# Optimization experiments

Hardware: AMD Instinct MI355X
Metric: run time of the kernel (lower is better)

## Reference

```python
import jax, jax.numpy as jnp
import numpy as np
import math

LN_EPS = 1e-5

def _ln(x, g, b):
    m = jnp.mean(x, -1, keepdims=True)
    v = jnp.mean((x - m) ** 2, -1, keepdims=True)
    return (x - m) / jnp.sqrt(v + LN_EPS) * g + b

def setup_inputs() -> dict:
    key = jax.random.key(0)
    ks = jax.random.split(key, 16)
    B, N, D, V = 2, 512, 128, 16
    w = lambda k, shape: jax.random.normal(k, shape, jnp.float32) * 0.02
    return {
        "scalar": jax.random.normal(ks[0], (B, N, D), jnp.float32),
        "vector": jax.random.normal(ks[1], (B, N, 3, V), jnp.float32),
        "coords": jax.random.normal(ks[2], (B, N, 3), jnp.float32),
        "w_q": w(ks[3], (D, D)), "b_q": jnp.zeros((D,), jnp.float32),
        "w_k": w(ks[4], (D, D)), "b_k": jnp.zeros((D,), jnp.float32),
        "w_v": w(ks[5], (D, D)), "b_v": jnp.zeros((D,), jnp.float32),
        "w_d1": w(ks[6], (1, D)), "b_d1": jnp.zeros((D,), jnp.float32),
        "w_d2": w(ks[7], (D, D)), "b_d2": jnp.zeros((D,), jnp.float32),
        "w_g": w(ks[8], (D, V)), "b_g": jnp.zeros((V,), jnp.float32),
        "w_o": w(ks[9], (D, D)), "b_o": jnp.zeros((D,), jnp.float32),
        "w_f1": w(ks[10], (D, 2 * D)), "b_f1": jnp.zeros((2 * D,), jnp.float32),
        "w_f2": w(ks[11], (2 * D, D)), "b_f2": jnp.zeros((D,), jnp.float32),
        "w_vo": w(ks[12], (V, V)), "b_vo": jnp.zeros((V,), jnp.float32),
        "g_s": jnp.ones((D,), jnp.float32), "be_s": jnp.zeros((D,), jnp.float32),
        "g_v": jnp.ones((V,), jnp.float32), "be_v": jnp.zeros((V,), jnp.float32),
    }

def reference(scalar, vector, coords, w_q, b_q, w_k, b_k, w_v, b_v,
              w_d1, b_d1, w_d2, b_d2, w_g, b_g, w_o, b_o,
              w_f1, b_f1, w_f2, b_f2, w_vo, b_vo, g_s, be_s, g_v, be_v):
    D = scalar.shape[-1]
    # pairwise geometry: [B,N,N,3], [B,N,N,1]
    rel = coords[:, :, None, :] - coords[:, None, :, :]
    dist = jnp.linalg.norm(rel, axis=-1, keepdims=True)
    direction = rel / jnp.maximum(dist, 1e-6)
    sn = _ln(scalar, g_s, be_s)
    q = sn @ w_q + b_q
    k = sn @ w_k + b_k
    v = sn @ w_v + b_v
    # distance-conditioned bias: [B,N,N,D]
    bias = jax.nn.gelu(dist @ w_d1 + b_d1, approximate=False) @ w_d2 + b_d2
    # q_i . (k_j + bias_ij) / sqrt(D)
    logits = (jnp.einsum('bid,bjd->bij', q, k)
              + jnp.einsum('bid,bijd->bij', q, bias)) / math.sqrt(D)
    attn = jax.nn.softmax(logits, axis=-1)
    # sum_j attn_ij * (v_j + bias_ij)
    upd = jnp.einsum('bij,bjd->bid', attn, v) + jnp.einsum('bij,bijd->bid', attn, bias)
    scalar = scalar + (upd @ w_o + b_o)
    h = _ln(scalar, g_s, be_s)
    scalar = scalar + (jax.nn.gelu(h @ w_f1 + b_f1, approximate=False) @ w_f2 + b_f2)
    gate = jax.nn.sigmoid(scalar @ w_g + b_g)  # [B,N,V]
    # sum_j attn_ij * (vector_j + dir_ij * gate_i) decomposed (same math, no BxNxNx3xV tensor)
    agg = (jnp.einsum('bij,bjcv->bicv', attn, vector)
           + jnp.einsum('bij,bijc->bic', attn, direction)[..., None] * gate[:, :, None, :])
    projected = _ln(agg, g_v, be_v) @ w_vo + b_vo
    return scalar, vector + projected
```

## Files before the change

kernel.cpp:

```cpp
#include <hip/hip_runtime.h>
#include <math.h>

#define D 128
#define F 256
#define V 16
#define NSEQ 512
#define NROW 1024
#define MQ 7

__device__ __forceinline__ float gelu_exact(float x) {
    return 0.5f * x * (1.0f + erff(x * 0.70710678118654752f));
}

__device__ __forceinline__ float waveSum(float v) {
#pragma unroll
    for (int o = 32; o; o >>= 1) v += __shfl_xor(v, o);
    return v;
}
__device__ __forceinline__ float waveMax(float v) {
#pragma unroll
    for (int o = 32; o; o >>= 1) v = fmaxf(v, __shfl_xor(v, o));
    return v;
}

__device__ __forceinline__ void build_A(const float* __restrict__ w_d1,
                                        const float* __restrict__ b_d1,
                                        float* A_s, int t) {
    if (t < D) {
        const float gam[MQ] = {0.f, 0.5f, 0.39894228f, 0.f, -0.06649038f, 0.f,
                               0.0099735570f};
        float w = w_d1[t], b = b_d1[t];
        float wp[MQ], bp[MQ];
        wp[0] = 1.f; bp[0] = 1.f;
#pragma unroll
        for (int i = 1; i < MQ; i++) { wp[i] = wp[i - 1] * w; bp[i] = bp[i - 1] * b; }
        float A[MQ];
#pragma unroll
        for (int m = 0; m < MQ; m++) A[m] = 0.f;
#pragma unroll
        for (int k = 1; k < MQ; k++) {
            float g = gam[k];
            if (g == 0.f) continue;
            float C = 1.f;
            for (int m = 0; m <= k; m++) {
                A[m] = fmaf(g * C, wp[m] * bp[k - m], A[m]);
                C = C * (float)(k - m) / (float)(m + 1);
            }
        }
#pragma unroll
        for (int m = 0; m < MQ; m++) A_s[t * MQ + m] = A[m];
    }
}

__global__ __launch_bounds__(1024) void k1_qkv(
    const float* __restrict__ scalar,
    const float* __restrict__ w_q, const float* __restrict__ b_q,
    const float* __restrict__ w_k, const float* __restrict__ b_k,
    const float* __restrict__ w_v, const float* __restrict__ b_v,
    const float* __restrict__ w_d1, const float* __restrict__ b_d1,
    const float* __restrict__ w_d2,
    const float* __restrict__ g_s, const float* __restrict__ be_s,
    float* __restrict__ qg, float* __restrict__ kTg, float* __restrict__ vg,
    float* __restrict__ Gg)
{
    const int t = threadIdx.x, h = t >> 8, u = t & 255, d = u & 127;
    const int w = t >> 6, ln = t & 63;
    const int r0 = blockIdx.x * 4, r = r0 + h;
    __shared__ float sn_s[4][D];
    __shared__ float k_s[4][D];
    __shared__ float pq[8][4][D], pk[8][4][D], pv[8][4][D];
    __shared__ float redA[16], redB[16];

    float x = scalar[(size_t)r * D + d];
    {
        float s = waveSum(x);
        if (ln == 0) redA[w] = s;
    }
    __syncthreads();
    float mean = (redA[4 * h] + redA[4 * h + 1] + redA[4 * h + 2] + redA[4 * h + 3])
               * (1.0f / 256.0f);
    float dv = x - mean;
    {
        float s = waveSum(dv * dv);
        if (ln == 0) redB[w] = s;
    }
    __syncthreads();
    float var = (redB[4 * h] + redB[4 * h + 1] + redB[4 * h + 2] + redB[4 * h + 3])
              * (1.0f / 256.0f);
    sn_s[h][d] = dv * rsqrtf(var + 1e-5f) * g_s[d] + be_s[d];
    __syncthreads();

    {
        const int eo = t >> 7, l = t & 127, e0 = eo * 16;
        float aq[4] = {0, 0, 0, 0}, ak[4] = {0, 0, 0, 0}, av[4] = {0, 0, 0, 0};
#pragma unroll 4
        for (int e = e0; e < e0 + 16; e++) {
            float wq = w_q[e * D + l], wk = w_k[e * D + l], wv = w_v[e * D + l];
#pragma unroll
            for (int rr = 0; rr < 4; rr++) {
                float s = sn_s[rr][e];
                aq[rr] = fmaf(s, wq, aq[rr]);
                ak[rr] = fmaf(s, wk, ak[rr]);
                av[rr] = fmaf(s, wv, av[rr]);
            }
        }
#pragma unroll
        for (int rr = 0; rr < 4; rr++) {
            pq[eo][rr][l] = aq[rr];
            pk[eo][rr][l] = ak[rr];
            pv[eo][rr][l] = av[rr];
        }
    }
    __syncthreads();

    for (int idx = t; idx < 1536; idx += 1024) {
        const int mat = idx >> 9, h2 = (idx >> 7) & 3, l = idx & 127;
        const float* P = (mat == 0) ? &pq[0][0][0]
                       : (mat == 1) ? &pk[0][0][0] : &pv[0][0][0];
        float acc = 0.f;
#pragma unroll
        for (int eo = 0; eo < 8; eo++) acc += P[(eo * 4 + h2) * D + l];
        if (mat == 0)      qg[(size_t)(r0 + h2) * D + l] = acc + b_q[l];
        else if (mat == 1) k_s[h2][l] = acc + b_k[l];
        else               vg[(size_t)(r0 + h2) * D + l] = acc + b_v[l];
    }
    __syncthreads();

    if (t < 512) kTg[(size_t)(t >> 2) * NROW + r0 + (t & 3)] = k_s[t & 3][t >> 2];

    if (blockIdx.x == 0) {
        float* A_s = &pq[0][0][0];
        build_A(w_d1, b_d1, A_s, t);
        __syncthreads();
        if (t < D * MQ) {
            const int m = t >> 7, l = t & 127;
            float acc = 0.f;
#pragma unroll 4
            for (int e = 0; e < D; e++)
                acc = fmaf(w_d2[e * D + l], A_s[e * MQ + m], acc);
            Gg[l * MQ + m] = acc;
        }
    }
}

__global__ __launch_bounds__(1024) void k23(
    const float* __restrict__ coords, const float* __restrict__ vecin,
    const float* __restrict__ scalar,
    const float* __restrict__ qg, const float* __restrict__ kTg,
    const float* __restrict__ vg, const float* __restrict__ Gg,
    const float* __restrict__ b_d2,
    const float* __restrict__ w_o, const float* __restrict__ b_o,
    const float* __restrict__ w_f1, const float* __restrict__ b_f1,
    const float* __restrict__ w_f2, const float* __restrict__ b_f2,
    const float* __restrict__ w_g, const float* __restrict__ b_g,
    const float* __restrict__ w_vo, const float* __restrict__ b_vo,
    const float* __restrict__ g_s, const float* __restrict__ be_s,
    const float* __restrict__ g_v, const float* __restrict__ be_v,
    float* __restrict__ out_s, float* __restrict__ out_v)
{
    const int t = threadIdx.x, h = t >> 8, u = t & 255;
    const int w = t >> 6, ln = t & 63;
    const int r0 = blockIdx.x * 4, r = r0 + h, b = r0 >> 9;
    __shared__ __align__(16) float q2_s[4][D];
    __shared__ float Gl_s[D * MQ];
    __shared__ float P_s[4][MQ];
    __shared__ __align__(16) float attn_s[4][NSEQ];
    __shared__ float scr[4096];
    __shared__ float avp[16][4][48];
    __shared__ float redA[16], redB[16];
    __shared__ float wredM[16][10];
    __shared__ float S_s[4][MQ], adir_s[4][3];
    __shared__ float upd_s[4][D], s1_s[4][D], h_s[4][D];
    __shared__ float t2_s[4][F];
    __shared__ float avec_s[4][48], gate_s[4][V], gp[8][4][V], lnv_s[4][48];

    if (t < 512) q2_s[t >> 7][t & 127] = qg[(size_t)(r0 + (t >> 7)) * D + (t & 127)];
    for (int idx = t; idx < D * MQ; idx += 1024) Gl_s[idx] = Gg[idx];

    const float cix = coords[(size_t)r * 3 + 0];
    const float ciy = coords[(size_t)r * 3 + 1];
    const float ciz = coords[(size_t)r * 3 + 2];
    const float2* cj2 = (const float2*)(coords + ((size_t)b * NSEQ + 2 * u) * 3);
    float2 ca = cj2[0], cb = cj2[1], cc = cj2[2];
    float rx0 = cix - ca.x, ry0 = ciy - ca.y, rz0 = ciz - cb.x;
    float rx1 = cix - cb.y, ry1 = ciy - cc.x, rz1 = ciz - cc.y;
    float d0 = sqrtf(rx0 * rx0 + ry0 * ry0 + rz0 * rz0);
    float d1 = sqrtf(rx1 * rx1 + ry1 * ry1 + rz1 * rz1);
    __syncthreads();

    {
        const int dd = u & 127;
        float qv = q2_s[h][dd];
        float pa[MQ];
#pragma unroll
        for (int m = 0; m < MQ; m++) pa[m] = qv * Gl_s[dd * MQ + m];
        pa[0] = fmaf(qv, b_d2[dd], pa[0]);
#pragma unroll
        for (int m = 0; m < MQ; m++) {
            float s = waveSum(pa[m]);
            if (ln == 0) wredM[w][m] = s;
        }
    }
    __syncthreads();
    if (t < 4 * MQ) {
        const int hh = t / MQ, m = t % MQ;
        P_s[hh][m] = (wredM[4 * hh][m] + wredM[4 * hh + 1][m]
                    + wredM[4 * hh + 2][m] + wredM[4 * hh + 3][m]) * 0.5f;
    }
    __syncthreads();

    float Pr[MQ];
#pragma unroll
    for (int m = 0; m < MQ; m++) Pr[m] = P_s[h][m];
    float s0 = 0.f, s1v = 0.f;
    {
        const float* kTe = kTg + (size_t)b * NSEQ + 2 * u;
        const float4* q4s = (const float4*)(&q2_s[h][0]);
#pragma unroll 8
        for (int e4 = 0; e4 < 32; e4++) {
            float4 qe = q4s[e4];
            float2 k0 = *(const float2*)(kTe + (size_t)(4 * e4 + 0) * NROW);
            float2 k1 = *(const float2*)(kTe + (size_t)(4 * e4 + 1) * NROW);
            float2 k2 = *(const float2*)(kTe + (size_t)(4 * e4 + 2) * NROW);
            float2 k3 = *(const float2*)(kTe + (size_t)(4 * e4 + 3) * NROW);
            s0 = fmaf(qe.x, k0.x, s0); s1v = fmaf(qe.x, k0.y, s1v);
            s0 = fmaf(qe.y, k1.x, s0); s1v = fmaf(qe.y, k1.y, s1v);
            s0 = fmaf(qe.z, k2.x, s0); s1v = fmaf(qe.z, k2.y, s1v);
            s0 = fmaf(qe.w, k3.x, s0); s1v = fmaf(qe.w, k3.y, s1v);
        }
    }
    const float sc = 0.08838834764831844f;
    float bias0 = Pr[MQ - 1], bias1 = Pr[MQ - 1];
#pragma unroll
    for (int m = MQ - 2; m >= 0; m--) {
        bias0 = fmaf(bias0, d0, Pr[m]);
        bias1 = fmaf(bias1, d1, Pr[m]);
    }
    float l0 = (s0 + bias0) * sc, l1 = (s1v + bias1) * sc;

    {
        float mx = waveMax(fmaxf(l0, l1));
        if (ln == 0) redA[w] = mx;
    }
    __syncthreads();
    float mx = fmaxf(fmaxf(redA[4 * h], redA[4 * h + 1]),
                     fmaxf(redA[4 * h + 2], redA[4 * h + 3]));
    float p0 = __expf(l0 - mx), p1 = __expf(l1 - mx);
    {
        float s = waveSum(p0 + p1);
        if (ln == 0) redB[w] = s;
    }
    __syncthreads();
    float inv = 1.0f / (redB[4 * h] + redB[4 * h + 1]
                      + redB[4 * h + 2] + redB[4 * h + 3]);
    float a0 = p0 * inv, a1 = p1 * inv;
    *(float2*)(&attn_s[h][2 * u]) = make_float2(a0, a1);

    {
        float red[10];
        float w0 = a0, w1 = a1;
#pragma unroll
        for (int m = 0; m < MQ; m++) { red[m] = w0 + w1; w0 *= d0; w1 *= d1; }
        float ia0 = a0 * __builtin_amdgcn_rcpf(fmaxf(d0, 1e-6f));
        float ia1 = a1 * __builtin_amdgcn_rcpf(fmaxf(d1, 1e-6f));
        red[7] = fmaf(ia0, rx0, ia1 * rx1);
        red[8] = fmaf(ia0, ry0, ia1 * ry1);
        red[9] = fmaf(ia0, rz0, ia1 * rz1);
#pragma unroll
        for (int m = 0; m < 10; m++) {
            float s = waveSum(red[m]);
            if (ln == 0) wredM[w][m] = s;
        }
    }
    __syncthreads();
    if (t < 40) {
        const int hh = t / 10, m = t % 10;
        float s = wredM[4 * hh][m] + wredM[4 * hh + 1][m]
                + wredM[4 * hh + 2][m] + wredM[4 * hh + 3][m];
        if (m < MQ) S_s[hh][m] = s;
        else        adir_s[hh][m - MQ] = s;
    }

    {
        const int dd = t & 127, jo = t >> 7, jb = 64 * jo;
        const float* vb = vg + ((size_t)b * NSEQ + jb) * D + dd;
        float c0 = 0.f, c1 = 0.f, c2 = 0.f, c3 = 0.f;
#pragma unroll 4
        for (int jj = 0; jj < 64; jj++) {
            float vv = vb[(size_t)jj * D];
            c0 = fmaf(attn_s[0][jb + jj], vv, c0);
            c1 = fmaf(attn_s[1][jb + jj], vv, c1);
            c2 = fmaf(attn_s[2][jb + jj], vv, c2);
            c3 = fmaf(attn_s[3][jb + jj], vv, c3);
        }
        scr[(jo * 4 + 0) * D + dd] = c0;
        scr[(jo * 4 + 1) * D + dd] = c1;
        scr[(jo * 4 + 2) * D + dd] = c2;
        scr[(jo * 4 + 3) * D + dd] = c3;
    }
    if (ln < 48) {
        const int jb = 32 * w;
        const float* vp = vecin + ((size_t)b * NSEQ + jb) * 48 + ln;
        float c0 = 0.f, c1 = 0.f, c2 = 0.f, c3 = 0.f;
#pragma unroll 4
        for (int jj = 0; jj < 32; jj++) {
            float vv = vp[(size_t)jj * 48];
            c0 = fmaf(attn_s[0][jb + jj], vv, c0);
            c1 = fmaf(attn_s[1][jb + jj], vv, c1);
            c2 = fmaf(attn_s[2][jb + jj], vv, c2);
            c3 = fmaf(attn_s[3][jb + jj], vv, c3);
        }
        avp[w][0][ln] = c0; avp[w][1][ln] = c1;
        avp[w][2][ln] = c2; avp[w][3][ln] = c3;
    }
    __syncthreads();

    if (t < 512) {
        const int hh = t >> 7, l = t & 127;
        float acc = 0.f;
#pragma unroll
        for (int jo = 0; jo < 8; jo++) acc += scr[(jo * 4 + hh) * D + l];
        float a = 0.f;
#pragma unroll
        for (int m = 0; m < MQ; m++) a = fmaf(Gl_s[l * MQ + m], S_s[hh][m], a);
        upd_s[hh][l] = acc + a + b_d2[l];
    } else if (t - 512 < 192) {
        const int idx = t - 512, hh = idx / 48, i2 = idx % 48;
        float s = 0.f;
#pragma unroll
        for (int w2 = 0; w2 < 16; w2++) s += avp[w2][hh][i2];
        avec_s[hh][i2] = s;
    }
    __syncthreads();

    {
        const int eo = t >> 7, l = t & 127, e0 = 16 * eo;
        float c0 = 0.f, c1 = 0.f, c2 = 0.f, c3 = 0.f;
#pragma unroll 4
        for (int e = e0; e < e0 + 16; e++) {
            float wv = w_o[e * D + l];
            c0 = fmaf(upd_s[0][e], wv, c0);
            c1 = fmaf(upd_s[1][e], wv, c1);
            c2 = fmaf(upd_s[2][e], wv, c2);
            c3 = fmaf(upd_s[3][e], wv, c3);
        }
        scr[(eo * 4 + 0) * D + l] = c0;
        scr[(eo * 4 + 1) * D + l] = c1;
        scr[(eo * 4 + 2) * D + l] = c2;
        scr[(eo * 4 + 3) * D + l] = c3;
    }
    __syncthreads();
    float xln = 0.f;
    {
        const int hh = (t >> 7) & 3, l = t & 127;
        if (t < 512) {
            float acc = 0.f;
#pragma unroll
            for (int eo = 0; eo < 8; eo++) acc += scr[(eo * 4 + hh) * D + l];
            xln = scalar[(size_t)(r0 + hh) * D + l] + acc + b_o[l];
            s1_s[hh][l] = xln;
        }
        float s = waveSum(xln);
        if (t < 512 && ln == 0) redA[w] = s;
    }
    __syncthreads();
    float dvv = 0.f;
    if (t < 512) {
        const int hh = (t >> 7) & 3;
        float mean = (redA[2 * hh] + redA[2 * hh + 1]) * (1.0f / 128.0f);
        dvv = xln - mean;
    }
    {
        float s = waveSum(dvv * dvv);
        if (t < 512 && ln == 0) redB[w] = s;
    }
    __syncthreads();
    if (t < 512) {
        const int hh = (t >> 7) & 3, l = t & 127;
        float var = (redB[2 * hh] + redB[2 * hh + 1]) * (1.0f / 128.0f);
        h_s[hh][l] = dvv * rsqrtf(var + 1e-5f) * g_s[l] + be_s[l];
    }
    __syncthreads();

    {
        const int f = t & 255, eq = t >> 8, e0 = 32 * eq;
        float c0 = 0.f, c1 = 0.f, c2 = 0.f, c3 = 0.f;
#pragma unroll 4
        for (int e = e0; e < e0 + 32; e++) {
            float wv = w_f1[e * F + f];
            c0 = fmaf(h_s[0][e], wv, c0);
            c1 = fmaf(h_s[1][e], wv, c1);
            c2 = fmaf(h_s[2][e], wv, c2);
            c3 = fmaf(h_s[3][e], wv, c3);
        }
        scr[(eq * 4 + 0) * F + f] = c0;
        scr[(eq * 4 + 1) * F + f] = c1;
        scr[(eq * 4 + 2) * F + f] = c2;
        scr[(eq * 4 + 3) * F + f] = c3;
    }
    __syncthreads();
    {
        const int hh = t >> 8, f = t & 255;
        t2_s[hh][f] = gelu_exact(scr[(0 * 4 + hh) * F + f] + scr[(1 * 4 + hh) * F + f]
                               + scr[(2 * 4 + hh) * F + f] + scr[(3 * 4 + hh) * F + f]
                               + b_f1[f]);
    }
    __syncthreads();

    {
        const int fo = t >> 7, l = t & 127, f0 = 32 * fo;
        float c0 = 0.f, c1 = 0.f, c2 = 0.f, c3 = 0.f;
#pragma unroll 4
        for (int f = f0; f < f0 + 32; f++) {
            float wv = w_f2[f * D + l];
            c0 = fmaf(t2_s[0][f], wv, c0);
            c1 = fmaf(t2_s[1][f], wv, c1);
            c2 = fmaf(t2_s[2][f], wv, c2);
            c3 = fmaf(t2_s[3][f], wv, c3);
        }
        scr[(fo * 4 + 0) * D + l] = c0;
        scr[(fo * 4 + 1) * D + l] = c1;
        scr[(fo * 4 + 2) * D + l] = c2;
        scr[(fo * 4 + 3) * D + l] = c3;
    }
    __syncthreads();
    if (t < 512) {
        const int hh = t >> 7, l = t & 127;
        float acc = 0.f;
#pragma unroll
        for (int fo = 0; fo < 8; fo++) acc += scr[(fo * 4 + hh) * D + l];
        float v2 = s1_s[hh][l] + acc + b_f2[l];
        out_s[(size_t)(r0 + hh) * D + l] = v2;
        s1_s[hh][l] = v2;
    }
    __syncthreads();

    if (t < 512) {
        const int dq = t >> 6, rr = (t >> 4) & 3, vv = t & 15, d2 = 16 * dq;
        float a = 0.f;
#pragma unroll 4
        for (int dd = d2; dd < d2 + 16; dd++)
            a = fmaf(s1_s[rr][dd], w_g[dd * V + vv], a);
        gp[dq][rr][vv] = a;
    }
    __syncthreads();
    if (t < 64) {
        const int rr = t >> 4, vv = t & 15;
        float a = b_g[vv];
#pragma unroll
        for (int dq = 0; dq < 8; dq++) a += gp[dq][rr][vv];
        gate_s[rr][vv] = 1.0f / (1.0f + __expf(-a));
    }
    __syncthreads();

    if (t < 192) {
        const int rr = t / 48, idx = t % 48, c = idx >> 4, vv = idx & 15;
        float agg = avec_s[rr][idx] + adir_s[rr][c] * gate_s[rr][vv];
        float s = agg;
#pragma unroll
        for (int o = 8; o; o >>= 1) s += __shfl_xor(s, o, 16);
        float mean = s * (1.0f / 16.0f);
        float e = agg - mean;
        float s2 = e * e;
#pragma unroll
        for (int o = 8; o; o >>= 1) s2 += __shfl_xor(s2, o, 16);
        float rstd = rsqrtf(s2 * (1.0f / 16.0f) + 1e-5f);
        lnv_s[rr][idx] = e * rstd * g_v[vv] + be_v[vv];
    }
    __syncthreads();
    if (t < 192) {
        const int rr = t / 48, idx = t % 48, c = idx >> 4, vv = idx & 15;
        const int row = r0 + rr;
        float a = b_vo[vv];
#pragma unroll
        for (int w2 = 0; w2 < V; w2++)
            a = fmaf(lnv_s[rr][c * V + w2], w_vo[w2 * V + vv], a);
        out_v[(size_t)row * 48 + idx] = vecin[(size_t)row * 48 + idx] + a;
    }
}

extern "C" void kernel_launch(void* const* d_in, const int* in_sizes, int n_in,
                              void* d_out, int out_size, void* d_ws, size_t ws_size,
                              hipStream_t stream)
{
    (void)in_sizes; (void)n_in; (void)out_size; (void)ws_size;
    const float* scalar = (const float*)d_in[0];
    const float* vecin  = (const float*)d_in[1];
    const float* coords = (const float*)d_in[2];
    const float* w_q  = (const float*)d_in[3];  const float* b_q  = (const float*)d_in[4];
    const float* w_k  = (const float*)d_in[5];  const float* b_k  = (const float*)d_in[6];
    const float* w_v  = (const float*)d_in[7];  const float* b_v  = (const float*)d_in[8];
    const float* w_d1 = (const float*)d_in[9];  const float* b_d1 = (const float*)d_in[10];
    const float* w_d2 = (const float*)d_in[11]; const float* b_d2 = (const float*)d_in[12];
    const float* w_g  = (const float*)d_in[13]; const float* b_g  = (const float*)d_in[14];
    const float* w_o  = (const float*)d_in[15]; const float* b_o  = (const float*)d_in[16];
    const float* w_f1 = (const float*)d_in[17]; const float* b_f1 = (const float*)d_in[18];
    const float* w_f2 = (const float*)d_in[19]; const float* b_f2 = (const float*)d_in[20];
    const float* w_vo = (const float*)d_in[21]; const float* b_vo = (const float*)d_in[22];
    const float* g_s  = (const float*)d_in[23]; const float* be_s = (const float*)d_in[24];
    const float* g_v  = (const float*)d_in[25]; const float* be_v = (const float*)d_in[26];

    float* ws = (float*)d_ws;
    float* qg  = ws;
    float* kTg = ws + 131072;
    float* vg  = ws + 262144;
    float* Gg  = ws + 393216;

    float* out_s = (float*)d_out;
    float* out_v = out_s + 131072;

    hipLaunchKernelGGL(k1_qkv, dim3(NROW / 4), dim3(1024), 0, stream,
                       scalar, w_q, b_q, w_k, b_k, w_v, b_v, w_d1, b_d1,
                       w_d2, g_s, be_s, qg, kTg, vg, Gg);
    hipLaunchKernelGGL(k23, dim3(NROW / 4), dim3(1024), 0, stream,
                       coords, vecin, scalar, qg, kTg, vg, Gg,
                       b_d2, w_o, b_o, w_f1, b_f1, w_f2, b_f2,
                       w_g, b_g, w_vo, b_vo, g_s, be_s, g_v, be_v,
                       out_s, out_v);
}
```

Before: 162.9 us.

## Fuse QKV and attention kernels into one cooperative launch with grid sync

Merges the two kernels into a single cooperative kernel that uses a grid-wide barrier between the QKV projection and the attention phase. Each block now keeps q in shared memory and recomputes the distance-bias polynomial coefficients locally, so they no longer round-trip through global memory. Small row-activation tiles are stored transposed so inner loops can read them as float4, and scratch buffers are folded into one shared array. The cost is a grid sync, redundant per-block build of the coefficients, and the requirement that all 256 blocks of 1024 threads be resident at once.

Result: slower. 215.8 us (+32.4%).

```diff
diff --git a/kernel.cpp b/kernel.cpp
--- a/kernel.cpp
+++ b/kernel.cpp
@@ -1,5 +1,8 @@
 #include <hip/hip_runtime.h>
+#include <hip/hip_cooperative_groups.h>
 #include <math.h>
+
+namespace cg = cooperative_groups;
 
 #define D 128
 #define F 256
@@ -52,103 +55,14 @@
     }
 }
 
-__global__ __launch_bounds__(1024) void k1_qkv(
-    const float* __restrict__ scalar,
+__global__ __launch_bounds__(1024) void fused(
+    const float* __restrict__ scalar, const float* __restrict__ vecin,
+    const float* __restrict__ coords,
     const float* __restrict__ w_q, const float* __restrict__ b_q,
     const float* __restrict__ w_k, const float* __restrict__ b_k,
     const float* __restrict__ w_v, const float* __restrict__ b_v,
     const float* __restrict__ w_d1, const float* __restrict__ b_d1,
-    const float* __restrict__ w_d2,
-    const float* __restrict__ g_s, const float* __restrict__ be_s,
-    float* __restrict__ qg, float* __restrict__ kTg, float* __restrict__ vg,
-    float* __restrict__ Gg)
-{
-    const int t = threadIdx.x, h = t >> 8, u = t & 255, d = u & 127;
-    const int w = t >> 6, ln = t & 63;
-    const int r0 = blockIdx.x * 4, r = r0 + h;
-    __shared__ float sn_s[4][D];
-    __shared__ float k_s[4][D];
-    __shared__ float pq[8][4][D], pk[8][4][D], pv[8][4][D];
-    __shared__ float redA[16], redB[16];
-
-    float x = scalar[(size_t)r * D + d];
-    {
-        float s = waveSum(x);
-        if (ln == 0) redA[w] = s;
-    }
-    __syncthreads();
-    float mean = (redA[4 * h] + redA[4 * h + 1] + redA[4 * h + 2] + redA[4 * h + 3])
-               * (1.0f / 256.0f);
-    float dv = x - mean;
-    {
-        float s = waveSum(dv * dv);
-        if (ln == 0) redB[w] = s;
-    }
-    __syncthreads();
-    float var = (redB[4 * h] + redB[4 * h + 1] + redB[4 * h + 2] + redB[4 * h + 3])
-              * (1.0f / 256.0f);
-    sn_s[h][d] = dv * rsqrtf(var + 1e-5f) * g_s[d] + be_s[d];
-    __syncthreads();
-
-    {
-        const int eo = t >> 7, l = t & 127, e0 = eo * 16;
-        float aq[4] = {0, 0, 0, 0}, ak[4] = {0, 0, 0, 0}, av[4] = {0, 0, 0, 0};
-#pragma unroll 4
-        for (int e = e0; e < e0 + 16; e++) {
-            float wq = w_q[e * D + l], wk = w_k[e * D + l], wv = w_v[e * D + l];
-#pragma unroll
-            for (int rr = 0; rr < 4; rr++) {
-                float s = sn_s[rr][e];
-                aq[rr] = fmaf(s, wq, aq[rr]);
-                ak[rr] = fmaf(s, wk, ak[rr]);
-                av[rr] = fmaf(s, wv, av[rr]);
-            }
-        }
-#pragma unroll
-        for (int rr = 0; rr < 4; rr++) {
-            pq[eo][rr][l] = aq[rr];
-            pk[eo][rr][l] = ak[rr];
-            pv[eo][rr][l] = av[rr];
-        }
-    }
-    __syncthreads();
-
-    for (int idx = t; idx < 1536; idx += 1024) {
-        const int mat = idx >> 9, h2 = (idx >> 7) & 3, l = idx & 127;
-        const float* P = (mat == 0) ? &pq[0][0][0]
-                       : (mat == 1) ? &pk[0][0][0] : &pv[0][0][0];
-        float acc = 0.f;
-#pragma unroll
-        for (int eo = 0; eo < 8; eo++) acc += P[(eo * 4 + h2) * D + l];
-        if (mat == 0)      qg[(size_t)(r0 + h2) * D + l] = acc + b_q[l];
-        else if (mat == 1) k_s[h2][l] = acc + b_k[l];
-        else               vg[(size_t)(r0 + h2) * D + l] = acc + b_v[l];
-    }
-    __syncthreads();
-
-    if (t < 512) kTg[(size_t)(t >> 2) * NROW + r0 + (t & 3)] = k_s[t & 3][t >> 2];
-
-    if (blockIdx.x == 0) {
-        float* A_s = &pq[0][0][0];
-        build_A(w_d1, b_d1, A_s, t);
-        __syncthreads();
-        if (t < D * MQ) {
-            const int m = t >> 7, l = t & 127;
-            float acc = 0.f;
-#pragma unroll 4
-            for (int e = 0; e < D; e++)
-                acc = fmaf(w_d2[e * D + l], A_s[e * MQ + m], acc);
-            Gg[l * MQ + m] = acc;
-        }
-    }
-}
-
-__global__ __launch_bounds__(1024) void k23(
-    const float* __restrict__ coords, const float* __restrict__ vecin,
-    const float* __restrict__ scalar,
-    const float* __restrict__ qg, const float* __restrict__ kTg,
-    const float* __restrict__ vg, const float* __restrict__ Gg,
-    const float* __restrict__ b_d2,
+    const float* __restrict__ w_d2, const float* __restrict__ b_d2,
     const float* __restrict__ w_o, const float* __restrict__ b_o,
     const float* __restrict__ w_f1, const float* __restrict__ b_f1,
     const float* __restrict__ w_f2, const float* __restrict__ b_f2,
@@ -156,79 +70,141 @@
     const float* __restrict__ w_vo, const float* __restrict__ b_vo,
     const float* __restrict__ g_s, const float* __restrict__ be_s,
     const float* __restrict__ g_v, const float* __restrict__ be_v,
+    float* __restrict__ kTg, float* __restrict__ vg,
     float* __restrict__ out_s, float* __restrict__ out_v)
 {
-    const int t = threadIdx.x, h = t >> 8, u = t & 255;
-    const int w = t >> 6, ln = t & 63;
+    const int t = threadIdx.x;
+    const int h = t >> 8, u = t & 255;
+    const int wvid = t >> 6, ln = t & 63;
     const int r0 = blockIdx.x * 4, r = r0 + h, b = r0 >> 9;
-    __shared__ __align__(16) float q2_s[4][D];
-    __shared__ float Gl_s[D * MQ];
-    __shared__ float P_s[4][MQ];
-    __shared__ __align__(16) float attn_s[4][NSEQ];
-    __shared__ float scr[4096];
-    __shared__ float avp[16][4][48];
-    __shared__ float redA[16], redB[16];
-    __shared__ float wredM[16][10];
-    __shared__ float S_s[4][MQ], adir_s[4][3];
-    __shared__ float upd_s[4][D], s1_s[4][D], h_s[4][D];
-    __shared__ float t2_s[4][F];
-    __shared__ float avec_s[4][48], gate_s[4][V], gp[8][4][V], lnv_s[4][48];
-
-    if (t < 512) q2_s[t >> 7][t & 127] = qg[(size_t)(r0 + (t >> 7)) * D + (t & 127)];
-    for (int idx = t; idx < D * MQ; idx += 1024) Gl_s[idx] = Gg[idx];
+
+    __shared__ __align__(16) float RA[12288];
+    __shared__ __align__(16) float qT[D][4];
+    __shared__ __align__(16) float snT[D][4];
+    __shared__ float k_s[4][D];
+    __shared__ float A_s[D * MQ];
+    __shared__ float G_s[D * MQ];
+    __shared__ __align__(16) float updT[D][4];
+    __shared__ __align__(16) float hT[D][4];
+    __shared__ __align__(16) float s1T[D][4];
+    __shared__ __align__(16) float t2T[F][4];
+    __shared__ float S_s[4][MQ], adir_s[4][3], avec_s[4][48], P_s[4][MQ];
+    __shared__ float redA[16], redB[16], wredM[16][10];
+    __shared__ float gate_s[4][V], gp[8][4][V], lnv_s[4][48];
+
+    build_A(w_d1, b_d1, A_s, t);
+
+    const int d = u & 127;
+    float x = scalar[(size_t)r * D + d];
+    { float s = waveSum(x); if (ln == 0) redA[wvid] = s; }
+    __syncthreads();
+    float mean = (redA[4 * h] + redA[4 * h + 1] + redA[4 * h + 2] + redA[4 * h + 3])
+               * (1.0f / 256.0f);
+    float dv = x - mean;
+    { float s = waveSum(dv * dv); if (ln == 0) redB[wvid] = s; }
+    __syncthreads();
+    float var = (redB[4 * h] + redB[4 * h + 1] + redB[4 * h + 2] + redB[4 * h + 3])
+              * (1.0f / 256.0f);
+    if (u < 128) snT[d][h] = dv * rsqrtf(var + 1e-5f) * g_s[d] + be_s[d];
+    __syncthreads();
+
+    {
+        const int eo = t >> 7, l = t & 127, e0 = eo * 16;
+        float aq[4] = {0, 0, 0, 0}, ak[4] = {0, 0, 0, 0}, av[4] = {0, 0, 0, 0};
+#pragma unroll 4
+        for (int e = e0; e < e0 + 16; e++) {
+            float4 s4 = *(const float4*)&snT[e][0];
+            float wq = w_q[e * D + l], wk = w_k[e * D + l], wvv = w_v[e * D + l];
+            aq[0] = fmaf(s4.x, wq, aq[0]); aq[1] = fmaf(s4.y, wq, aq[1]);
+            aq[2] = fmaf(s4.z, wq, aq[2]); aq[3] = fmaf(s4.w, wq, aq[3]);
+            ak[0] = fmaf(s4.x, wk, ak[0]); ak[1] = fmaf(s4.y, wk, ak[1]);
+            ak[2] = fmaf(s4.z, wk, ak[2]); ak[3] = fmaf(s4.w, wk, ak[3]);
+            av[0] = fmaf(s4.x, wvv, av[0]); av[1] = fmaf(s4.y, wvv, av[1]);
+            av[2] = fmaf(s4.z, wvv, av[2]); av[3] = fmaf(s4.w, wvv, av[3]);
+        }
+#pragma unroll
+        for (int rr = 0; rr < 4; rr++) {
+            RA[eo * 512 + rr * 128 + l] = aq[rr];
+            RA[4096 + eo * 512 + rr * 128 + l] = ak[rr];
+            RA[8192 + eo * 512 + rr * 128 + l] = av[rr];
+        }
+    }
+    __syncthreads();
+    for (int idx = t; idx < 1536; idx += 1024) {
+        const int mat = idx >> 9, h2 = (idx >> 7) & 3, l = idx & 127;
+        const float* P = RA + mat * 4096;
+        float acc = 0.f;
+#pragma unroll
+        for (int eo = 0; eo < 8; eo++) acc += P[eo * 512 + h2 * 128 + l];
+        if (mat == 0)      qT[l][h2] = acc + b_q[l];
+        else if (mat == 1) k_s[h2][l] = acc + b_k[l];
+        else               vg[(size_t)(r0 + h2) * D + l] = acc + b_v[l];
+    }
+    __syncthreads();
+    if (t < 512) kTg[(size_t)(t >> 2) * NROW + r0 + (t & 3)] = k_s[t & 3][t >> 2];
+
+    if (t < D * MQ) {
+        const int m = t >> 7, l = t & 127;
+        float acc = 0.f;
+#pragma unroll 4
+        for (int e = 0; e < D; e++)
+            acc = fmaf(w_d2[e * D + l], A_s[e * MQ + m], acc);
+        G_s[l * MQ + m] = acc;
+    }
+    __syncthreads();
+
+    {
+        float qv2 = qT[d][h];
+        float pa[MQ];
+#pragma unroll
+        for (int m = 0; m < MQ; m++) pa[m] = qv2 * G_s[d * MQ + m];
+        pa[0] = fmaf(qv2, b_d2[d], pa[0]);
+#pragma unroll
+        for (int m = 0; m < MQ; m++) {
+            float s = waveSum(pa[m]);
+            if (ln == 0) wredM[wvid][m] = s;
+        }
+    }
+    __syncthreads();
+    if (t < 4 * MQ) {
+        const int hh = t / MQ, m = t % MQ;
+        P_s[hh][m] = (wredM[4 * hh][m] + wredM[4 * hh + 1][m]
+                    + wredM[4 * hh + 2][m] + wredM[4 * hh + 3][m]) * 0.5f;
+    }
 
     const float cix = coords[(size_t)r * 3 + 0];
     const float ciy = coords[(size_t)r * 3 + 1];
     const float ciz = coords[(size_t)r * 3 + 2];
     const float2* cj2 = (const float2*)(coords + ((size_t)b * NSEQ + 2 * u) * 3);
-    float2 ca = cj2[0], cb = cj2[1], cc = cj2[2];
-    float rx0 = cix - ca.x, ry0 = ciy - ca.y, rz0 = ciz - cb.x;
-    float rx1 = cix - cb.y, ry1 = ciy - cc.x, rz1 = ciz - cc.y;
+    float2 ca = cj2[0], cb2 = cj2[1], cc = cj2[2];
+    float rx0 = cix - ca.x, ry0 = ciy - ca.y, rz0 = ciz - cb2.x;
+    float rx1 = cix - cb2.y, ry1 = ciy - cc.x, rz1 = ciz - cc.y;
     float d0 = sqrtf(rx0 * rx0 + ry0 * ry0 + rz0 * rz0);
     float d1 = sqrtf(rx1 * rx1 + ry1 * ry1 + rz1 * rz1);
-    __syncthreads();
-
-    {
-        const int dd = u & 127;
-        float qv = q2_s[h][dd];
-        float pa[MQ];
-#pragma unroll
-        for (int m = 0; m < MQ; m++) pa[m] = qv * Gl_s[dd * MQ + m];
-        pa[0] = fmaf(qv, b_d2[dd], pa[0]);
-#pragma unroll
-        for (int m = 0; m < MQ; m++) {
-            float s = waveSum(pa[m]);
-            if (ln == 0) wredM[w][m] = s;
-        }
-    }
-    __syncthreads();
-    if (t < 4 * MQ) {
-        const int hh = t / MQ, m = t % MQ;
-        P_s[hh][m] = (wredM[4 * hh][m] + wredM[4 * hh + 1][m]
-                    + wredM[4 * hh + 2][m] + wredM[4 * hh + 3][m]) * 0.5f;
-    }
-    __syncthreads();
-
+
+    cg::this_grid().sync();
+
+    {
+        const int jj = t & 511, eh = t >> 9;
+        const float* ke = kTg + (size_t)(64 * eh) * NROW + (size_t)b * NSEQ + jj;
+        float c0 = 0.f, c1 = 0.f, c2 = 0.f, c3 = 0.f;
+#pragma unroll 4
+        for (int e = 0; e < 64; e++) {
+            float kv2 = ke[(size_t)e * NROW];
+            float4 q4 = *(const float4*)&qT[64 * eh + e][0];
+            c0 = fmaf(q4.x, kv2, c0); c1 = fmaf(q4.y, kv2, c1);
+            c2 = fmaf(q4.z, kv2, c2); c3 = fmaf(q4.w, kv2, c3);
+        }
+        *(float4*)&RA[2048 + (eh * 512 + jj) * 4] = make_float4(c0, c1, c2, c3);
+    }
+    __syncthreads();
+
+    const int j0 = 2 * u, j1 = 2 * u + 1;
+    float qk0 = RA[2048 + j0 * 4 + h] + RA[4096 + j0 * 4 + h];
+    float qk1 = RA[2048 + j1 * 4 + h] + RA[4096 + j1 * 4 + h];
     float Pr[MQ];
 #pragma unroll
     for (int m = 0; m < MQ; m++) Pr[m] = P_s[h][m];
-    float s0 = 0.f, s1v = 0.f;
-    {
-        const float* kTe = kTg + (size_t)b * NSEQ + 2 * u;
-        const float4* q4s = (const float4*)(&q2_s[h][0]);
-#pragma unroll 8
-        for (int e4 = 0; e4 < 32; e4++) {
-            float4 qe = q4s[e4];
-            float2 k0 = *(const float2*)(kTe + (size_t)(4 * e4 + 0) * NROW);
-            float2 k1 = *(const float2*)(kTe + (size_t)(4 * e4 + 1) * NROW);
-            float2 k2 = *(const float2*)(kTe + (size_t)(4 * e4 + 2) * NROW);
-            float2 k3 = *(const float2*)(kTe + (size_t)(4 * e4 + 3) * NROW);
-            s0 = fmaf(qe.x, k0.x, s0); s1v = fmaf(qe.x, k0.y, s1v);
-            s0 = fmaf(qe.y, k1.x, s0); s1v = fmaf(qe.y, k1.y, s1v);
-            s0 = fmaf(qe.z, k2.x, s0); s1v = fmaf(qe.z, k2.y, s1v);
-            s0 = fmaf(qe.w, k3.x, s0); s1v = fmaf(qe.w, k3.y, s1v);
-        }
-    }
     const float sc = 0.08838834764831844f;
     float bias0 = Pr[MQ - 1], bias1 = Pr[MQ - 1];
 #pragma unroll
@@ -236,11 +212,10 @@
         bias0 = fmaf(bias0, d0, Pr[m]);
         bias1 = fmaf(bias1, d1, Pr[m]);
     }
-    float l0 = (s0 + bias0) * sc, l1 = (s1v + bias1) * sc;
-
+    float l0 = (qk0 + bias0) * sc, l1 = (qk1 + bias1) * sc;
     {
         float mx = waveMax(fmaxf(l0, l1));
-        if (ln == 0) redA[w] = mx;
+        if (ln == 0) redA[wvid] = mx;
     }
     __syncthreads();
     float mx = fmaxf(fmaxf(redA[4 * h], redA[4 * h + 1]),
@@ -248,13 +223,14 @@
     float p0 = __expf(l0 - mx), p1 = __expf(l1 - mx);
     {
         float s = waveSum(p0 + p1);
-        if (ln == 0) redB[w] = s;
+        if (ln == 0) redB[wvid] = s;
     }
     __syncthreads();
     float inv = 1.0f / (redB[4 * h] + redB[4 * h + 1]
                       + redB[4 * h + 2] + redB[4 * h + 3]);
     float a0 = p0 * inv, a1 = p1 * inv;
-    *(float2*)(&attn_s[h][2 * u]) = make_float2(a0, a1);
+    RA[j0 * 4 + h] = a0;
+    RA[j1 * 4 + h] = a1;
 
     {
         float red[10];
@@ -269,7 +245,7 @@
 #pragma unroll
         for (int m = 0; m < 10; m++) {
             float s = waveSum(red[m]);
-            if (ln == 0) wredM[w][m] = s;
+            if (ln == 0) wredM[wvid][m] = s;
         }
     }
     __syncthreads();
@@ -287,31 +263,31 @@
         float c0 = 0.f, c1 = 0.f, c2 = 0.f, c3 = 0.f;
 #pragma unroll 4
         for (int jj = 0; jj < 64; jj++) {
-            float vv = vb[(size_t)jj * D];
-            c0 = fmaf(attn_s[0][jb + jj], vv, c0);
-            c1 = fmaf(attn_s[1][jb + jj], vv, c1);
-            c2 = fmaf(attn_s[2][jb + jj], vv, c2);
-            c3 = fmaf(attn_s[3][jb + jj], vv, c3);
-        }
-        scr[(jo * 4 + 0) * D + dd] = c0;
-        scr[(jo * 4 + 1) * D + dd] = c1;
-        scr[(jo * 4 + 2) * D + dd] = c2;
-        scr[(jo * 4 + 3) * D + dd] = c3;
+            float4 at = *(const float4*)&RA[(jb + jj) * 4];
+            float vv2 = vb[(size_t)jj * D];
+            c0 = fmaf(at.x, vv2, c0); c1 = fmaf(at.y, vv2, c1);
+            c2 = fmaf(at.z, vv2, c2); c3 = fmaf(at.w, vv2, c3);
+        }
+        RA[2048 + (jo * 4 + 0) * 128 + dd] = c0;
+        RA[2048 + (jo * 4 + 1) * 128 + dd] = c1;
+        RA[2048 + (jo * 4 + 2) * 128 + dd] = c2;
+        RA[2048 + (jo * 4 + 3) * 128 + dd] = c3;
     }
     if (ln < 48) {
-        const int jb = 32 * w;
+        const int jb = 32 * wvid;
         const float* vp = vecin + ((size_t)b * NSEQ + jb) * 48 + ln;
         float c0 = 0.f, c1 = 0.f, c2 = 0.f, c3 = 0.f;
 #pragma unroll 4
         for (int jj = 0; jj < 32; jj++) {
-            float vv = vp[(size_t)jj * 48];
-            c0 = fmaf(attn_s[0][jb + jj], vv, c0);
-            c1 = fmaf(attn_s[1][jb + jj], vv, c1);
-            c2 = fmaf(attn_s[2][jb + jj], vv, c2);
-            c3 = fmaf(attn_s[3][jb + jj], vv, c3);
-        }
-        avp[w][0][ln] = c0; avp[w][1][ln] = c1;
-        avp[w][2][ln] = c2; avp[w][3][ln] = c3;
+            float4 at = *(const float4*)&RA[(jb + jj) * 4];
+            float vv2 = vp[(size_t)jj * 48];
+            c0 = fmaf(at.x, vv2, c0); c1 = fmaf(at.y, vv2, c1);
+            c2 = fmaf(at.z, vv2, c2); c3 = fmaf(at.w, vv2, c3);
+        }
+        RA[6144 + (wvid * 4 + 0) * 48 + ln] = c0;
+        RA[6144 + (wvid * 4 + 1) * 48 + ln] = c1;
+        RA[6144 + (wvid * 4 + 2) * 48 + ln] = c2;
+        RA[6144 + (wvid * 4 + 3) * 48 + ln] = c3;
     }
     __syncthreads();
 
@@ -319,16 +295,16 @@
         const int hh = t >> 7, l = t & 127;
         float acc = 0.f;
 #pragma unroll
-        for (int jo = 0; jo < 8; jo++) acc += scr[(jo * 4 + hh) * D + l];
+        for (int jo = 0; jo < 8; jo++) acc += RA[2048 + (jo * 4 + hh) * 128 + l];
         float a = 0.f;
 #pragma unroll
-        for (int m = 0; m < MQ; m++) a = fmaf(Gl_s[l * MQ + m], S_s[hh][m], a);
-        upd_s[hh][l] = acc + a + b_d2[l];
+        for (int m = 0; m < MQ; m++) a = fmaf(G_s[l * MQ + m], S_s[hh][m], a);
+        updT[l][hh] = acc + a + b_d2[l];
     } else if (t - 512 < 192) {
         const int idx = t - 512, hh = idx / 48, i2 = idx % 48;
         float s = 0.f;
 #pragma unroll
-        for (int w2 = 0; w2 < 16; w2++) s += avp[w2][hh][i2];
+        for (int w2 = 0; w2 < 16; w2++) s += RA[6144 + (w2 * 4 + hh) * 48 + i2];
         avec_s[hh][i2] = s;
     }
     __syncthreads();
@@ -338,16 +314,15 @@
         float c0 = 0.f, c1 = 0.f, c2 = 0.f, c3 = 0.f;
 #pragma unroll 4
         for (int e = e0; e < e0 + 16; e++) {
-            float wv = w_o[e * D + l];
-            c0 = fmaf(upd_s[0][e], wv, c0);
-            c1 = fmaf(upd_s[1][e], wv, c1);
-            c2 = fmaf(upd_s[2][e], wv, c2);
-            c3 = fmaf(upd_s[3][e], wv, c3);
-        }
-        scr[(eo * 4 + 0) * D + l] = c0;
-        scr[(eo * 4 + 1) * D + l] = c1;
-        scr[(eo * 4 + 2) * D + l] = c2;
-        scr[(eo * 4 + 3) * D + l] = c3;
+            float4 up = *(const float4*)&updT[e][0];
+            float wv2 = w_o[e * D + l];
+            c0 = fmaf(up.x, wv2, c0); c1 = fmaf(up.y, wv2, c1);
+            c2 = fmaf(up.z, wv2, c2); c3 = fmaf(up.w, wv2, c3);
+        }
+        RA[2048 + (eo * 4 + 0) * 128 + l] = c0;
+        RA[2048 + (eo * 4 + 1) * 128 + l] = c1;
+        RA[2048 + (eo * 4 + 2) * 128 + l] = c2;
+        RA[2048 + (eo * 4 + 3) * 128 + l] = c3;
     }
     __syncthreads();
     float xln = 0.f;
@@ -356,29 +331,29 @@
         if (t < 512) {
             float acc = 0.f;
 #pragma unroll
-            for (int eo = 0; eo < 8; eo++) acc += scr[(eo * 4 + hh) * D + l];
+            for (int eo = 0; eo < 8; eo++) acc += RA[2048 + (eo * 4 + hh) * 128 + l];
             xln = scalar[(size_t)(r0 + hh) * D + l] + acc + b_o[l];
-            s1_s[hh][l] = xln;
+            s1T[l][hh] = xln;
         }
         float s = waveSum(xln);
-        if (t < 512 && ln == 0) redA[w] = s;
+        if (t < 512 && ln == 0) redA[wvid] = s;
     }
     __syncthreads();
     float dvv = 0.f;
     if (t < 512) {
         const int hh = (t >> 7) & 3;
-        float mean = (redA[2 * hh] + redA[2 * hh + 1]) * (1.0f / 128.0f);
-        dvv = xln - mean;
+        float mean2 = (redA[2 * hh] + redA[2 * hh + 1]) * (1.0f / 128.0f);
+        dvv = xln - mean2;
     }
     {
         float s = waveSum(dvv * dvv);
-        if (t < 512 && ln == 0) redB[w] = s;
+        if (t < 512 && ln == 0) redB[wvid] = s;
     }
     __syncthreads();
     if (t < 512) {
         const int hh = (t >> 7) & 3, l = t & 127;
-        float var = (redB[2 * hh] + redB[2 * hh + 1]) * (1.0f / 128.0f);
-        h_s[hh][l] = dvv * rsqrtf(var + 1e-5f) * g_s[l] + be_s[l];
+        float var2 = (redB[2 * hh] + redB[2 * hh + 1]) * (1.0f / 128.0f);
+        hT[l][hh] = dvv * rsqrtf(var2 + 1e-5f) * g_s[l] + be_s[l];
     }
     __syncthreads();
 
@@ -387,23 +362,23 @@
         float c0 = 0.f, c1 = 0.f, c2 = 0.f, c3 = 0.f;
 #pragma unroll 4
         for (int e = e0; e < e0 + 32; e++) {
-            float wv = w_f1[e * F + f];
-            c0 = fmaf(h_s[0][e], wv, c0);
-            c1 = fmaf(h_s[1][e], wv, c1);
-            c2 = fmaf(h_s[2][e], wv, c2);
-            c3 = fmaf(h_s[3][e], wv, c3);
-        }
-        scr[(eq * 4 + 0) * F + f] = c0;
-        scr[(eq * 4 + 1) * F + f] = c1;
-        scr[(eq * 4 + 2) * F + f] = c2;
-        scr[(eq * 4 + 3) * F + f] = c3;
+            float4 hv = *(const float4*)&hT[e][0];
+            float wv2 = w_f1[e * F + f];
+            c0 = fmaf(hv.x, wv2, c0); c1 = fmaf(hv.y, wv2, c1);
+            c2 = fmaf(hv.z, wv2, c2); c3 = fmaf(hv.w, wv2, c3);
+        }
+        RA[2048 + (eq * 4 + 0) * F + f] = c0;
+        RA[2048 + (eq * 4 + 1) * F + f] = c1;
+        RA[2048 + (eq * 4 + 2) * F + f] = c2;
+        RA[2048 + (eq * 4 + 3) * F + f] = c3;
     }
     __syncthreads();
     {
         const int hh = t >> 8, f = t & 255;
-        t2_s[hh][f] = gelu_exact(scr[(0 * 4 + hh) * F + f] + scr[(1 * 4 + hh) * F + f]
-                               + scr[(2 * 4 + hh) * F + f] + scr[(3 * 4 + hh) * F + f]
-                               + b_f1[f]);
+        t2T[f][hh] = gelu_exact(RA[2048 + (0 * 4 + hh) * F + f]
+                              + RA[2048 + (1 * 4 + hh) * F + f]
+                              + RA[2048 + (2 * 4 + hh) * F + f]
+                              + RA[2048 + (3 * 4 + hh) * F + f] + b_f1[f]);
     }
     __syncthreads();
 
@@ -412,26 +387,25 @@
         float c0 = 0.f, c1 = 0.f, c2 = 0.f, c3 = 0.f;
 #pragma unroll 4
         for (int f = f0; f < f0 + 32; f++) {
-            float wv = w_f2[f * D + l];
-            c0 = fmaf(t2_s[0][f], wv, c0);
-            c1 = fmaf(t2_s[1][f], wv, c1);
-            c2 = fmaf(t2_s[2][f], wv, c2);
-            c3 = fmaf(t2_s[3][f], wv, c3);
-        }
-        scr[(fo * 4 + 0) * D + l] = c0;
-        scr[(fo * 4 + 1) * D + l] = c1;
-        scr[(fo * 4 + 2) * D + l] = c2;
-        scr[(fo * 4 + 3) * D + l] = c3;
+            float4 tv = *(const float4*)&t2T[f][0];
+            float wv2 = w_f2[f * D + l];
+            c0 = fmaf(tv.x, wv2, c0); c1 = fmaf(tv.y, wv2, c1);
+            c2 = fmaf(tv.z, wv2, c2); c3 = fmaf(tv.w, wv2, c3);
+        }
+        RA[2048 + (fo * 4 + 0) * 128 + l] = c0;
+        RA[2048 + (fo * 4 + 1) * 128 + l] = c1;
+        RA[2048 + (fo * 4 + 2) * 128 + l] = c2;
+        RA[2048 + (fo * 4 + 3) * 128 + l] = c3;
     }
     __syncthreads();
     if (t < 512) {
         const int hh = t >> 7, l = t & 127;
         float acc = 0.f;
 #pragma unroll
-        for (int fo = 0; fo < 8; fo++) acc += scr[(fo * 4 + hh) * D + l];
-        float v2 = s1_s[hh][l] + acc + b_f2[l];
+        for (int fo = 0; fo < 8; fo++) acc += RA[2048 + (fo * 4 + hh) * 128 + l];
+        float v2 = s1T[l][hh] + acc + b_f2[l];
         out_s[(size_t)(r0 + hh) * D + l] = v2;
-        s1_s[hh][l] = v2;
+        s1T[l][hh] = v2;
     }
     __syncthreads();
 
@@ -440,7 +414,7 @@
         float a = 0.f;
 #pragma unroll 4
         for (int dd = d2; dd < d2 + 16; dd++)
-            a = fmaf(s1_s[rr][dd], w_g[dd * V + vv], a);
+            a = fmaf(s1T[dd][rr], w_g[dd * V + vv], a);
         gp[dq][rr][vv] = a;
     }
     __syncthreads();
@@ -459,8 +433,8 @@
         float s = agg;
 #pragma unroll
         for (int o = 8; o; o >>= 1) s += __shfl_xor(s, o, 16);
-        float mean = s * (1.0f / 16.0f);
-        float e = agg - mean;
+        float mean2 = s * (1.0f / 16.0f);
+        float e = agg - mean2;
         float s2 = e * e;
 #pragma unroll
         for (int o = 8; o; o >>= 1) s2 += __shfl_xor(s2, o, 16);
@@ -500,21 +474,23 @@
     const float* g_s  = (const float*)d_in[23]; const float* be_s = (const float*)d_in[24];
     const float* g_v  = (const float*)d_in[25]; const float* be_v = (const float*)d_in[26];
 
-    float* ws = (float*)d_ws;
-    float* qg  = ws;
-    float* kTg = ws + 131072;
-    float* vg  = ws + 262144;
-    float* Gg  = ws + 393216;
+    float* ws  = (float*)d_ws;
+    float* kTg = ws;
+    float* vg  = ws + 131072;
 
     float* out_s = (float*)d_out;
     float* out_v = out_s + 131072;
 
-    hipLaunchKernelGGL(k1_qkv, dim3(NROW / 4), dim3(1024), 0, stream,
-                       scalar, w_q, b_q, w_k, b_k, w_v, b_v, w_d1, b_d1,
-                       w_d2, g_s, be_s, qg, kTg, vg, Gg);
-    hipLaunchKernelGGL(k23, dim3(NROW / 4), dim3(1024), 0, stream,
-                       coords, vecin, scalar, qg, kTg, vg, Gg,
-                       b_d2, w_o, b_o, w_f1, b_f1, w_f2, b_f2,
-                       w_g, b_g, w_vo, b_vo, g_s, be_s, g_v, be_v,
-                       out_s, out_v);
-}
+    void* args[] = {
+        (void*)&scalar, (void*)&vecin, (void*)&coords,
+        (void*)&w_q, (void*)&b_q, (void*)&w_k, (void*)&b_k,
+        (void*)&w_v, (void*)&b_v, (void*)&w_d1, (void*)&b_d1,
+        (void*)&w_d2, (void*)&b_d2, (void*)&w_o, (void*)&b_o,
+        (void*)&w_f1, (void*)&b_f1, (void*)&w_f2, (void*)&b_f2,
+        (void*)&w_g, (void*)&b_g, (void*)&w_vo, (void*)&b_vo,
+        (void*)&g_s, (void*)&be_s, (void*)&g_v, (void*)&be_v,
+        (void*)&kTg, (void*)&vg, (void*)&out_s, (void*)&out_v };
+
+    hipLaunchCooperativeKernel((const void*)fused, dim3(NROW / 4), dim3(1024),
+                               args, 0u, stream);
+}
```
